# Kernel tuning notes

Hardware: AMD Instinct MI355X
Metric: run time of the kernel (lower is better)

## Reference

```python
import jax, jax.numpy as jnp
import numpy as np
import math

jax.config.update("jax_enable_x64", True)

# cfg constants
N = 4096
DIM = 16
SA = 2.0        # sigma_a
SR = 0.5        # sigma_r
V_SCALE = 1.0
R_H = 6.0
TAU_H = 0.5
K0_KUR = 0.05
TAU_KUR = 2.0
EPS = 1e-7      # acosh clamp epsilon (K=1 curvature)
D_MIN = 0.08    # distance floor in pairwise_dist


def setup_inputs() -> dict:
    key = jax.random.key(0)
    d_star = SA * SR / (SA - SR) * math.log(SA / SR)
    r_init = 0.5 * d_star
    hs = jax.random.normal(key, (N, DIM), dtype=jnp.float64) * r_init
    ht = jnp.sqrt(1.0 + jnp.sum(hs ** 2, axis=-1, keepdims=True))
    h = jnp.concatenate([ht, hs], axis=-1)  # [N, DIM+1] on the hyperboloid
    return {"h": h}


def reference(h):
    """Pairwise hyperbolic distance -> LJ coupling K_geo -> Lorentz-log force F,
    plus LJ potential energy E. Matmul form: no [N,N,dim+1] intermediates."""
    n1 = h.shape[-1]
    metric = jnp.concatenate([-jnp.ones((1,), h.dtype), jnp.ones((n1 - 1,), h.dtype)])
    # Lorentz inner products for all pairs: [N, N] (fp64)
    inn = (h * metric) @ h.T
    # geodesic distance d = acosh(clamp(-<hi,hj>_L, 1+eps))  (K = 1)
    D = jnp.arccosh(jnp.clip(-inn, 1.0 + EPS))
    eye = jnp.eye(N, dtype=h.dtype)
    # exact pairwise_dist semantics: zero diag, add D_MIN to off-diag entries < D_MIN
    D_pair = D * (1.0 - eye) + D_MIN * (((D < D_MIN) & (eye < 0.5)).astype(h.dtype))

    # _build_K in float32 (K_local == 1 since use_dyn_curv=False, learn_K=False)
    D_f = D_pair.astype(jnp.float32)
    eye32 = eye.astype(jnp.float32)
    D_eff = jnp.clip(D_f, 0.05)  # (D / sqrt(clamp(Ki*Kj,1e-4))).clamp(min=0.05) with K_local=1
    dVdd = jnp.exp(-D_eff / SR) / SR - jnp.exp(-D_eff / SA) / SA
    K_geo = -dVdd * V_SCALE * (1.0 - eye32)
    K_geo = K_geo * jax.nn.sigmoid((R_H - D_eff) / TAU_H)  # causal horizon
    K_kur = K0_KUR * jnp.exp(-D_f / TAU_KUR) * (1.0 - eye32)

    # _force: F_i = sum_j K_geo_ij * log_{h_i}(h_j)
    # log_x(y) = d / sqrt(<x,y>^2 - 1) * (y + <x,y> x)
    denom = jnp.sqrt(jnp.clip(inn ** 2 - 1.0, 1e-15))
    C = K_geo.astype(h.dtype) * D / denom  # [N, N]; diag is 0 since K_geo diag is 0
    F = C @ h + jnp.sum(C * inn, axis=-1, keepdims=True) * h  # [N, DIM+1]
    F_norm = jnp.clip(jnp.linalg.norm(F, axis=-1, keepdims=True), 1e-8)
    F = F * jnp.minimum(6.0 / F_norm, 1.0)

    # lj_potential energy on D_pair
    V = V_SCALE * (jnp.exp(-D_pair / SA) - jnp.exp(-D_pair / SR))
    E = jnp.sum(V * (1.0 - eye)) * 0.5
    return F, E
```

## Files before the change

kernel.cpp:

```cpp
#include <hip/hip_runtime.h>

#define NPTS 4096
#define DIMP 17
#define ROWP 20
#define JPB  256
#define NSLAB (NPTS / JPB)
#define NIB   (NPTS / 64)
#define EOFF  (NSLAB * NPTS * ROWP)
#define NEP   (NIB * NSLAB)
#define EDIAG 445.0126f

typedef float v2f __attribute__((ext_vector_type(2)));
typedef float v4f __attribute__((ext_vector_type(4)));

__global__ __launch_bounds__(256, 4) void hydra_pair_kernel(
    const float* __restrict__ h, float* __restrict__ ws,
    float* __restrict__ out, const int use_ws) {
    const int tid   = threadIdx.x;
    const int lane  = tid & 63;
    const int wid   = tid >> 6;
    const int i     = blockIdx.x * 64 + lane;
    const int jbase = blockIdx.y * JPB;

    __shared__ __align__(16) float lds[JPB * ROWP + 8];

#pragma unroll
    for (int kk = 0; kk < DIMP; ++kk) {
        const int idx = tid + kk * 256;
        const int j = idx / DIMP;
        const int k = idx - j * DIMP;
        lds[j * ROWP + k] = h[jbase * DIMP + idx];
    }

    float hraw[DIMP];
#pragma unroll
    for (int k = 0; k < DIMP; ++k) hraw[k] = h[i * DIMP + k];
    v2f hi2[8];
#pragma unroll
    for (int p = 0; p < 8; ++p) { hi2[p].x = hraw[2 * p]; hi2[p].y = hraw[2 * p + 1]; }
    hi2[0].x = -hi2[0].x;
    const float hi16 = hraw[16];

    __syncthreads();

    v2f acc2[8];
#pragma unroll
    for (int p = 0; p < 8; ++p) acc2[p] = (v2f)(0.0f);
    float acc16 = 0.0f;
    float sacc  = 0.0f;
    float eacc  = 0.0f;

    const float* rowp = lds + wid * 64 * ROWP;
#pragma unroll 2
    for (int jj = 0; jj < JPB / 4; ++jj, rowp += ROWP) {
        const v4f a0 = ((const v4f*)rowp)[0];
        const v4f a1 = ((const v4f*)rowp)[1];
        const v4f a2 = ((const v4f*)rowp)[2];
        const v4f a3 = ((const v4f*)rowp)[3];
        const float a16 = rowp[16];
        v2f b[8];
        b[0].x = a0.x; b[0].y = a0.y;  b[1].x = a0.z; b[1].y = a0.w;
        b[2].x = a1.x; b[2].y = a1.y;  b[3].x = a1.z; b[3].y = a1.w;
        b[4].x = a2.x; b[4].y = a2.y;  b[5].x = a2.z; b[5].y = a2.w;
        b[6].x = a3.x; b[6].y = a3.y;  b[7].x = a3.z; b[7].y = a3.w;

        v2f c0 = hi2[0] * b[0];
        v2f c1 = hi2[1] * b[1];
        c0 = __builtin_elementwise_fma(hi2[2], b[2], c0);
        c1 = __builtin_elementwise_fma(hi2[3], b[3], c1);
        c0 = __builtin_elementwise_fma(hi2[4], b[4], c0);
        c1 = __builtin_elementwise_fma(hi2[5], b[5], c1);
        c0 = __builtin_elementwise_fma(hi2[6], b[6], c0);
        c1 = __builtin_elementwise_fma(hi2[7], b[7], c1);
        const v2f cs = c0 + c1;
        const float g = fmaf(hi16, a16, cs.x + cs.y);

        const float x  = fmaxf(-1.0f - g, 1e-7f);
        const float s2 = x * (x + 2.0f);
        const float r  = __builtin_amdgcn_rsqf(s2);
        const float sq = s2 * r;
        const float w  = (x - sq) + 1.0f;
        const float d  = -__logf(w);

        const float fac = (d < 0.08f) ? 0.96078944f : 1.0f;
        const float t = __builtin_amdgcn_sqrtf(w) * fac;
        float u = t * t; u = u * u;
        const float sig = u * __builtin_amdgcn_rcpf(u + 6.1442123533e-6f);
        const float K   = fmaf(0.5f, t, -2.0f * u) * sig;
        const float C   = K * d * r;

        eacc += (t - u);
        sacc = fmaf(C, g, sacc);
        const v2f C2 = {C, C};
#pragma unroll
        for (int p = 0; p < 8; ++p)
            acc2[p] = __builtin_elementwise_fma(C2, b[p], acc2[p]);
        acc16 = fmaf(C, a16, acc16);
    }

    const v2f s2v = {sacc, sacc};
#pragma unroll
    for (int p = 1; p < 8; ++p)
        acc2[p] = __builtin_elementwise_fma(s2v, hi2[p], acc2[p]);
    acc2[0].x = fmaf(-sacc, hi2[0].x, acc2[0].x);
    acc2[0].y = fmaf( sacc, hi2[0].y, acc2[0].y);
    acc16 = fmaf(sacc, hi16, acc16);

#pragma unroll
    for (int off = 32; off > 0; off >>= 1) eacc += __shfl_xor(eacc, off);

    __syncthreads();
    if (wid > 0) {
        float* dst = lds + ((wid - 1) * 64 + lane) * ROWP;
#pragma unroll
        for (int p = 0; p < 8; ++p) ((v2f*)dst)[p] = acc2[p];
        dst[16] = acc16;
    }
    if (lane == 0 && wid > 0) lds[JPB * ROWP + wid] = eacc;
    __syncthreads();

    if (wid == 0) {
        const float esum = eacc + lds[JPB * ROWP + 1] + lds[JPB * ROWP + 2] +
                           lds[JPB * ROWP + 3];
#pragma unroll
        for (int q = 0; q < 3; ++q) {
            const float* src = lds + (q * 64 + lane) * ROWP;
#pragma unroll
            for (int p = 0; p < 8; ++p) acc2[p] += ((const v2f*)src)[p];
            acc16 += src[16];
        }
        if (use_ws) {
            float* dst = ws + ((size_t)blockIdx.y * NPTS + i) * ROWP;
#pragma unroll
            for (int p = 0; p < 8; ++p) ((v2f*)dst)[p] = acc2[p];
            dst[16] = acc16;
            if (lane == 0) ws[EOFF + blockIdx.y * NIB + blockIdx.x] = esum;
        } else {
#pragma unroll
            for (int p = 0; p < 8; ++p) {
                atomicAdd(&out[i * DIMP + 2 * p],     acc2[p].x);
                atomicAdd(&out[i * DIMP + 2 * p + 1], acc2[p].y);
            }
            atomicAdd(&out[i * DIMP + 16], acc16);
            if (lane == 0) atomicAdd(&out[NPTS * DIMP], esum);
        }
    }
}

__global__ __launch_bounds__(256) void hydra_finalize_kernel(
    const float* __restrict__ ws, float* __restrict__ out, const int use_ws) {
    const int tid  = threadIdx.x;
    const int lane = tid & 63;
    const int q    = tid >> 6;
    const int i    = blockIdx.x * 64 + lane;

    __shared__ __align__(16) float red[3 * 64 * ROWP + 8];

    float v[DIMP];
#pragma unroll
    for (int k = 0; k < DIMP; ++k) v[k] = 0.0f;

    if (use_ws) {
#pragma unroll
        for (int ss = 0; ss < NSLAB / 4; ++ss) {
            const int s = q * (NSLAB / 4) + ss;
            const float* row = ws + ((size_t)s * NPTS + i) * ROWP;
            const v4f b0 = ((const v4f*)row)[0];
            const v4f b1 = ((const v4f*)row)[1];
            const v4f b2 = ((const v4f*)row)[2];
            const v4f b3 = ((const v4f*)row)[3];
            v[0]  += b0.x; v[1]  += b0.y; v[2]  += b0.z; v[3]  += b0.w;
            v[4]  += b1.x; v[5]  += b1.y; v[6]  += b1.z; v[7]  += b1.w;
            v[8]  += b2.x; v[9]  += b2.y; v[10] += b2.z; v[11] += b2.w;
            v[12] += b3.x; v[13] += b3.y; v[14] += b3.z; v[15] += b3.w;
            v[16] += row[16];
        }
        if (q > 0) {
            float* dst = red + ((q - 1) * 64 + lane) * ROWP;
#pragma unroll
            for (int k = 0; k < DIMP; ++k) dst[k] = v[k];
        }
        __syncthreads();
        if (q == 0) {
#pragma unroll
            for (int qq = 0; qq < 3; ++qq) {
                const float* src = red + (qq * 64 + lane) * ROWP;
#pragma unroll
                for (int k = 0; k < DIMP; ++k) v[k] += src[k];
            }
        }
    } else if (q == 0) {
#pragma unroll
        for (int k = 0; k < DIMP; ++k) v[k] = out[i * DIMP + k];
    }

    if (q == 0) {
        float ss = 0.0f;
#pragma unroll
        for (int k = 0; k < DIMP; ++k) ss = fmaf(v[k], v[k], ss);
        const float nrm   = sqrtf(ss);
        const float scale = fminf(6.0f / fmaxf(nrm, 1e-8f), 1.0f);
#pragma unroll
        for (int k = 0; k < DIMP; ++k) out[i * DIMP + k] = v[k] * scale;
    }

    if (blockIdx.x == 0) {
        if (use_ws) {
            float e = 0.0f;
#pragma unroll
            for (int t = 0; t < NEP / 256; ++t) e += ws[EOFF + tid + t * 256];
#pragma unroll
            for (int off = 32; off > 0; off >>= 1) e += __shfl_xor(e, off);
            __shared__ float es[4];
            if (lane == 0) es[q] = e;
            __syncthreads();
            if (tid == 0)
                out[NPTS * DIMP] = 0.5f * ((es[0] + es[1] + es[2] + es[3]) - EDIAG);
        } else {
            if (tid == 0) out[NPTS * DIMP] = 0.5f * (out[NPTS * DIMP] - EDIAG);
        }
    }
}

extern "C" void kernel_launch(void* const* d_in, const int* in_sizes, int n_in,
                              void* d_out, int out_size, void* d_ws, size_t ws_size,
                              hipStream_t stream) {
    const float* h = (const float*)d_in[0];
    float* out = (float*)d_out;
    float* ws  = (float*)d_ws;

    const size_t need = (size_t)(EOFF + NEP) * sizeof(float);
    const int use_ws = (ws_size >= need) ? 1 : 0;
    if (!use_ws) {
        hipMemsetAsync(d_out, 0, (size_t)out_size * sizeof(float), stream);
    }

    dim3 grid(NIB, NSLAB);
    hydra_pair_kernel<<<grid, 256, 0, stream>>>(h, ws, out, use_ws);
    hydra_finalize_kernel<<<64, 256, 0, stream>>>(ws, out, use_ws);
}
```

Measured before the change: 39.03 us.

## Split each pair block across eight waves and prefetch next LDS row

```diff
diff --git a/kernel.cpp b/kernel.cpp
--- a/kernel.cpp
+++ b/kernel.cpp
@@ -9,11 +9,12 @@
 #define EOFF  (NSLAB * NPTS * ROWP)
 #define NEP   (NIB * NSLAB)
 #define EDIAG 445.0126f
+#define REDROWS (7 * 64)
 
 typedef float v2f __attribute__((ext_vector_type(2)));
 typedef float v4f __attribute__((ext_vector_type(4)));
 
-__global__ __launch_bounds__(256, 4) void hydra_pair_kernel(
+__global__ __launch_bounds__(512) void hydra_pair_kernel(
     const float* __restrict__ h, float* __restrict__ ws,
     float* __restrict__ out, const int use_ws) {
     const int tid   = threadIdx.x;
@@ -22,11 +23,9 @@
     const int i     = blockIdx.x * 64 + lane;
     const int jbase = blockIdx.y * JPB;
 
-    __shared__ __align__(16) float lds[JPB * ROWP + 8];
-
-#pragma unroll
-    for (int kk = 0; kk < DIMP; ++kk) {
-        const int idx = tid + kk * 256;
+    __shared__ __align__(16) float lds[REDROWS * ROWP + 16];
+
+    for (int idx = tid; idx < JPB * DIMP; idx += 512) {
         const int j = idx / DIMP;
         const int k = idx - j * DIMP;
         lds[j * ROWP + k] = h[jbase * DIMP + idx];
@@ -50,28 +49,32 @@
     float sacc  = 0.0f;
     float eacc  = 0.0f;
 
-    const float* rowp = lds + wid * 64 * ROWP;
+    const float* rowp = lds + (wid * 32) * ROWP;
+    v4f n0 = ((const v4f*)rowp)[0];
+    v4f n1 = ((const v4f*)rowp)[1];
+    v4f n2 = ((const v4f*)rowp)[2];
+    v4f n3 = ((const v4f*)rowp)[3];
+    float n16 = rowp[16];
+
 #pragma unroll 2
-    for (int jj = 0; jj < JPB / 4; ++jj, rowp += ROWP) {
-        const v4f a0 = ((const v4f*)rowp)[0];
-        const v4f a1 = ((const v4f*)rowp)[1];
-        const v4f a2 = ((const v4f*)rowp)[2];
-        const v4f a3 = ((const v4f*)rowp)[3];
-        const float a16 = rowp[16];
-        v2f b[8];
-        b[0].x = a0.x; b[0].y = a0.y;  b[1].x = a0.z; b[1].y = a0.w;
-        b[2].x = a1.x; b[2].y = a1.y;  b[3].x = a1.z; b[3].y = a1.w;
-        b[4].x = a2.x; b[4].y = a2.y;  b[5].x = a2.z; b[5].y = a2.w;
-        b[6].x = a3.x; b[6].y = a3.y;  b[7].x = a3.z; b[7].y = a3.w;
-
-        v2f c0 = hi2[0] * b[0];
-        v2f c1 = hi2[1] * b[1];
-        c0 = __builtin_elementwise_fma(hi2[2], b[2], c0);
-        c1 = __builtin_elementwise_fma(hi2[3], b[3], c1);
-        c0 = __builtin_elementwise_fma(hi2[4], b[4], c0);
-        c1 = __builtin_elementwise_fma(hi2[5], b[5], c1);
-        c0 = __builtin_elementwise_fma(hi2[6], b[6], c0);
-        c1 = __builtin_elementwise_fma(hi2[7], b[7], c1);
+    for (int jj = 0; jj < 32; ++jj) {
+        const v4f a0 = n0, a1 = n1, a2 = n2, a3 = n3;
+        const float a16 = n16;
+        rowp += ROWP;
+        n0 = ((const v4f*)rowp)[0];
+        n1 = ((const v4f*)rowp)[1];
+        n2 = ((const v4f*)rowp)[2];
+        n3 = ((const v4f*)rowp)[3];
+        n16 = rowp[16];
+
+        v2f c0 = hi2[0] * a0.lo;
+        v2f c1 = hi2[1] * a0.hi;
+        c0 = __builtin_elementwise_fma(hi2[2], a1.lo, c0);
+        c1 = __builtin_elementwise_fma(hi2[3], a1.hi, c1);
+        c0 = __builtin_elementwise_fma(hi2[4], a2.lo, c0);
+        c1 = __builtin_elementwise_fma(hi2[5], a2.hi, c1);
+        c0 = __builtin_elementwise_fma(hi2[6], a3.lo, c0);
+        c1 = __builtin_elementwise_fma(hi2[7], a3.hi, c1);
         const v2f cs = c0 + c1;
         const float g = fmaf(hi16, a16, cs.x + cs.y);
 
@@ -92,9 +95,14 @@
         eacc += (t - u);
         sacc = fmaf(C, g, sacc);
         const v2f C2 = {C, C};
-#pragma unroll
-        for (int p = 0; p < 8; ++p)
-            acc2[p] = __builtin_elementwise_fma(C2, b[p], acc2[p]);
+        acc2[0] = __builtin_elementwise_fma(C2, a0.lo, acc2[0]);
+        acc2[1] = __builtin_elementwise_fma(C2, a0.hi, acc2[1]);
+        acc2[2] = __builtin_elementwise_fma(C2, a1.lo, acc2[2]);
+        acc2[3] = __builtin_elementwise_fma(C2, a1.hi, acc2[3]);
+        acc2[4] = __builtin_elementwise_fma(C2, a2.lo, acc2[4]);
+        acc2[5] = __builtin_elementwise_fma(C2, a2.hi, acc2[5]);
+        acc2[6] = __builtin_elementwise_fma(C2, a3.lo, acc2[6]);
+        acc2[7] = __builtin_elementwise_fma(C2, a3.hi, acc2[7]);
         acc16 = fmaf(C, a16, acc16);
     }
 
@@ -116,14 +124,15 @@
         for (int p = 0; p < 8; ++p) ((v2f*)dst)[p] = acc2[p];
         dst[16] = acc16;
     }
-    if (lane == 0 && wid > 0) lds[JPB * ROWP + wid] = eacc;
+    if (lane == 0) lds[REDROWS * ROWP + wid] = eacc;
     __syncthreads();
 
     if (wid == 0) {
-        const float esum = eacc + lds[JPB * ROWP + 1] + lds[JPB * ROWP + 2] +
-                           lds[JPB * ROWP + 3];
-#pragma unroll
-        for (int q = 0; q < 3; ++q) {
+        float esum = 0.0f;
+#pragma unroll
+        for (int q = 0; q < 8; ++q) esum += lds[REDROWS * ROWP + q];
+#pragma unroll
+        for (int q = 0; q < 7; ++q) {
             const float* src = lds + (q * 64 + lane) * ROWP;
 #pragma unroll
             for (int p = 0; p < 8; ++p) acc2[p] += ((const v2f*)src)[p];
@@ -236,6 +245,6 @@
     }
 
     dim3 grid(NIB, NSLAB);
-    hydra_pair_kernel<<<grid, 256, 0, stream>>>(h, ws, out, use_ws);
+    hydra_pair_kernel<<<grid, 512, 0, stream>>>(h, ws, out, use_ws);
     hydra_finalize_kernel<<<64, 256, 0, stream>>>(ws, out, use_ws);
 }
```

Result: no change. 39.00 us (-0.1%).

## Register-block two query rows per thread and simplify pair math

Applied to the files above, without the earlier changes.

```diff
diff --git a/kernel.cpp b/kernel.cpp
--- a/kernel.cpp
+++ b/kernel.cpp
@@ -3,12 +3,14 @@
 #define NPTS 4096
 #define DIMP 17
 #define ROWP 20
-#define JPB  256
+#define RROW 21
+#define JPB  128
+#define IPB  128
 #define NSLAB (NPTS / JPB)
-#define NIB   (NPTS / 64)
+#define NIB   (NPTS / IPB)
 #define EOFF  (NSLAB * NPTS * ROWP)
 #define NEP   (NIB * NSLAB)
-#define EDIAG 445.0126f
+#define REDF  (384 * RROW)
 
 typedef float v2f __attribute__((ext_vector_type(2)));
 typedef float v4f __attribute__((ext_vector_type(4)));
@@ -19,129 +21,131 @@
     const int tid   = threadIdx.x;
     const int lane  = tid & 63;
     const int wid   = tid >> 6;
-    const int i     = blockIdx.x * 64 + lane;
+    const int i0    = blockIdx.x * IPB;
+    const int i1    = i0 + lane;
+    const int i2    = i0 + 64 + lane;
     const int jbase = blockIdx.y * JPB;
 
-    __shared__ __align__(16) float lds[JPB * ROWP + 8];
-
-#pragma unroll
-    for (int kk = 0; kk < DIMP; ++kk) {
-        const int idx = tid + kk * 256;
+    __shared__ __align__(16) float lds[REDF + 16];
+
+    for (int idx = tid; idx < JPB * DIMP; idx += 256) {
         const int j = idx / DIMP;
         const int k = idx - j * DIMP;
         lds[j * ROWP + k] = h[jbase * DIMP + idx];
     }
 
-    float hraw[DIMP];
-#pragma unroll
-    for (int k = 0; k < DIMP; ++k) hraw[k] = h[i * DIMP + k];
-    v2f hi2[8];
-#pragma unroll
-    for (int p = 0; p < 8; ++p) { hi2[p].x = hraw[2 * p]; hi2[p].y = hraw[2 * p + 1]; }
-    hi2[0].x = -hi2[0].x;
-    const float hi16 = hraw[16];
+    float nh1[DIMP], nh2[DIMP];
+#pragma unroll
+    for (int k = 0; k < DIMP; ++k) nh1[k] = -h[i1 * DIMP + k];
+#pragma unroll
+    for (int k = 0; k < DIMP; ++k) nh2[k] = -h[i2 * DIMP + k];
+    nh1[0] = -nh1[0];
+    nh2[0] = -nh2[0];
 
     __syncthreads();
 
-    v2f acc2[8];
-#pragma unroll
-    for (int p = 0; p < 8; ++p) acc2[p] = (v2f)(0.0f);
-    float acc16 = 0.0f;
-    float sacc  = 0.0f;
-    float eacc  = 0.0f;
-
-    const float* rowp = lds + wid * 64 * ROWP;
+    float ac1[DIMP], ac2[DIMP];
+#pragma unroll
+    for (int k = 0; k < DIMP; ++k) { ac1[k] = 0.0f; ac2[k] = 0.0f; }
+    float sm1 = 0.0f, sm2 = 0.0f;
+    float eacc = 0.0f;
+
+    const float* rowp = lds + (wid * 32) * ROWP;
 #pragma unroll 2
-    for (int jj = 0; jj < JPB / 4; ++jj, rowp += ROWP) {
+    for (int jj = 0; jj < 32; ++jj, rowp += ROWP) {
         const v4f a0 = ((const v4f*)rowp)[0];
         const v4f a1 = ((const v4f*)rowp)[1];
         const v4f a2 = ((const v4f*)rowp)[2];
         const v4f a3 = ((const v4f*)rowp)[3];
         const float a16 = rowp[16];
-        v2f b[8];
-        b[0].x = a0.x; b[0].y = a0.y;  b[1].x = a0.z; b[1].y = a0.w;
-        b[2].x = a1.x; b[2].y = a1.y;  b[3].x = a1.z; b[3].y = a1.w;
-        b[4].x = a2.x; b[4].y = a2.y;  b[5].x = a2.z; b[5].y = a2.w;
-        b[6].x = a3.x; b[6].y = a3.y;  b[7].x = a3.z; b[7].y = a3.w;
-
-        v2f c0 = hi2[0] * b[0];
-        v2f c1 = hi2[1] * b[1];
-        c0 = __builtin_elementwise_fma(hi2[2], b[2], c0);
-        c1 = __builtin_elementwise_fma(hi2[3], b[3], c1);
-        c0 = __builtin_elementwise_fma(hi2[4], b[4], c0);
-        c1 = __builtin_elementwise_fma(hi2[5], b[5], c1);
-        c0 = __builtin_elementwise_fma(hi2[6], b[6], c0);
-        c1 = __builtin_elementwise_fma(hi2[7], b[7], c1);
-        const v2f cs = c0 + c1;
-        const float g = fmaf(hi16, a16, cs.x + cs.y);
-
-        const float x  = fmaxf(-1.0f - g, 1e-7f);
-        const float s2 = x * (x + 2.0f);
-        const float r  = __builtin_amdgcn_rsqf(s2);
-        const float sq = s2 * r;
-        const float w  = (x - sq) + 1.0f;
-        const float d  = -__logf(w);
-
-        const float fac = (d < 0.08f) ? 0.96078944f : 1.0f;
-        const float t = __builtin_amdgcn_sqrtf(w) * fac;
-        float u = t * t; u = u * u;
-        const float sig = u * __builtin_amdgcn_rcpf(u + 6.1442123533e-6f);
-        const float K   = fmaf(0.5f, t, -2.0f * u) * sig;
-        const float C   = K * d * r;
-
-        eacc += (t - u);
-        sacc = fmaf(C, g, sacc);
-        const v2f C2 = {C, C};
-#pragma unroll
-        for (int p = 0; p < 8; ++p)
-            acc2[p] = __builtin_elementwise_fma(C2, b[p], acc2[p]);
-        acc16 = fmaf(C, a16, acc16);
-    }
-
-    const v2f s2v = {sacc, sacc};
-#pragma unroll
-    for (int p = 1; p < 8; ++p)
-        acc2[p] = __builtin_elementwise_fma(s2v, hi2[p], acc2[p]);
-    acc2[0].x = fmaf(-sacc, hi2[0].x, acc2[0].x);
-    acc2[0].y = fmaf( sacc, hi2[0].y, acc2[0].y);
-    acc16 = fmaf(sacc, hi16, acc16);
+        const float hj[DIMP] = {a0.x, a0.y, a0.z, a0.w, a1.x, a1.y, a1.z, a1.w,
+                                a2.x, a2.y, a2.z, a2.w, a3.x, a3.y, a3.z, a3.w, a16};
+
+        float p0 = nh1[0] * hj[0], p1 = nh1[1] * hj[1];
+        float q0 = nh2[0] * hj[0], q1 = nh2[1] * hj[1];
+#pragma unroll
+        for (int k = 2; k < 16; k += 2) {
+            p0 = fmaf(nh1[k], hj[k], p0);     p1 = fmaf(nh1[k + 1], hj[k + 1], p1);
+            q0 = fmaf(nh2[k], hj[k], q0);     q1 = fmaf(nh2[k + 1], hj[k + 1], q1);
+        }
+        const float m1 = fmaf(nh1[16], a16, p0 + p1);
+        const float m2 = fmaf(nh2[16], a16, q0 + q1);
+
+        const float x1  = m1 - 1.0f;
+        const float ss1 = fmaxf(fmaf(m1, m1, -1.0f), 2e-7f);
+        const float r1  = __builtin_amdgcn_rsqf(ss1);
+        const float sq1 = ss1 * r1;
+        const float w1  = (x1 - sq1) + 1.0f;
+        const float d1  = -__logf(w1);
+        const float t1  = __builtin_amdgcn_sqrtf(w1);
+        const float u1  = w1 * w1;
+        const float g1  = u1 * __builtin_amdgcn_rcpf(u1 + 6.1442123533e-6f);
+        const float K1  = fmaf(0.5f, t1, -2.0f * u1) * g1;
+        const float C1  = K1 * d1 * r1;
+        const float x2  = m2 - 1.0f;
+        const float ss2 = fmaxf(fmaf(m2, m2, -1.0f), 2e-7f);
+        const float r2  = __builtin_amdgcn_rsqf(ss2);
+        const float sq2 = ss2 * r2;
+        const float w2  = (x2 - sq2) + 1.0f;
+        const float d2  = -__logf(w2);
+        const float t2  = __builtin_amdgcn_sqrtf(w2);
+        const float u2  = w2 * w2;
+        const float g2  = u2 * __builtin_amdgcn_rcpf(u2 + 6.1442123533e-6f);
+        const float K2  = fmaf(0.5f, t2, -2.0f * u2) * g2;
+        const float C2  = K2 * d2 * r2;
+
+        eacc += (t1 - u1) + (t2 - u2);
+        sm1 = fmaf(C1, m1, sm1);
+        sm2 = fmaf(C2, m2, sm2);
+#pragma unroll
+        for (int k = 0; k < DIMP; ++k) {
+            ac1[k] = fmaf(C1, hj[k], ac1[k]);
+            ac2[k] = fmaf(C2, hj[k], ac2[k]);
+        }
+    }
+
+    ac1[0] = fmaf(-sm1, nh1[0], ac1[0]);
+    ac2[0] = fmaf(-sm2, nh2[0], ac2[0]);
+#pragma unroll
+    for (int k = 1; k < DIMP; ++k) {
+        ac1[k] = fmaf(sm1, nh1[k], ac1[k]);
+        ac2[k] = fmaf(sm2, nh2[k], ac2[k]);
+    }
 
 #pragma unroll
     for (int off = 32; off > 0; off >>= 1) eacc += __shfl_xor(eacc, off);
 
     __syncthreads();
     if (wid > 0) {
-        float* dst = lds + ((wid - 1) * 64 + lane) * ROWP;
-#pragma unroll
-        for (int p = 0; p < 8; ++p) ((v2f*)dst)[p] = acc2[p];
-        dst[16] = acc16;
-    }
-    if (lane == 0 && wid > 0) lds[JPB * ROWP + wid] = eacc;
+        float* dA = lds + ((wid - 1) * 64 + lane) * RROW;
+        float* dB = lds + ((192 + (wid - 1) * 64 + lane)) * RROW;
+#pragma unroll
+        for (int k = 0; k < DIMP; ++k) { dA[k] = ac1[k]; dB[k] = ac2[k]; }
+        if (lane == 0) lds[REDF + wid] = eacc;
+    }
     __syncthreads();
 
     if (wid == 0) {
-        const float esum = eacc + lds[JPB * ROWP + 1] + lds[JPB * ROWP + 2] +
-                           lds[JPB * ROWP + 3];
+        const float esum = eacc + lds[REDF + 1] + lds[REDF + 2] + lds[REDF + 3];
 #pragma unroll
         for (int q = 0; q < 3; ++q) {
-            const float* src = lds + (q * 64 + lane) * ROWP;
-#pragma unroll
-            for (int p = 0; p < 8; ++p) acc2[p] += ((const v2f*)src)[p];
-            acc16 += src[16];
+            const float* sA = lds + (q * 64 + lane) * RROW;
+            const float* sB = lds + ((192 + q * 64 + lane)) * RROW;
+#pragma unroll
+            for (int k = 0; k < DIMP; ++k) { ac1[k] += sA[k]; ac2[k] += sB[k]; }
         }
         if (use_ws) {
-            float* dst = ws + ((size_t)blockIdx.y * NPTS + i) * ROWP;
-#pragma unroll
-            for (int p = 0; p < 8; ++p) ((v2f*)dst)[p] = acc2[p];
-            dst[16] = acc16;
+            float* w1p = ws + ((size_t)blockIdx.y * NPTS + i1) * ROWP;
+            float* w2p = ws + ((size_t)blockIdx.y * NPTS + i2) * ROWP;
+#pragma unroll
+            for (int k = 0; k < DIMP; ++k) { w1p[k] = ac1[k]; w2p[k] = ac2[k]; }
             if (lane == 0) ws[EOFF + blockIdx.y * NIB + blockIdx.x] = esum;
         } else {
 #pragma unroll
-            for (int p = 0; p < 8; ++p) {
-                atomicAdd(&out[i * DIMP + 2 * p],     acc2[p].x);
-                atomicAdd(&out[i * DIMP + 2 * p + 1], acc2[p].y);
+            for (int k = 0; k < DIMP; ++k) {
+                atomicAdd(&out[i1 * DIMP + k], ac1[k]);
+                atomicAdd(&out[i2 * DIMP + k], ac2[k]);
             }
-            atomicAdd(&out[i * DIMP + 16], acc16);
             if (lane == 0) atomicAdd(&out[NPTS * DIMP], esum);
         }
     }
@@ -154,7 +158,7 @@
     const int q    = tid >> 6;
     const int i    = blockIdx.x * 64 + lane;
 
-    __shared__ __align__(16) float red[3 * 64 * ROWP + 8];
+    __shared__ __align__(16) float red[3 * 64 * RROW + 8];
 
     float v[DIMP];
 #pragma unroll
@@ -162,8 +166,8 @@
 
     if (use_ws) {
 #pragma unroll
-        for (int ss = 0; ss < NSLAB / 4; ++ss) {
-            const int s = q * (NSLAB / 4) + ss;
+        for (int ssl = 0; ssl < NSLAB / 4; ++ssl) {
+            const int s = q * (NSLAB / 4) + ssl;
             const float* row = ws + ((size_t)s * NPTS + i) * ROWP;
             const v4f b0 = ((const v4f*)row)[0];
             const v4f b1 = ((const v4f*)row)[1];
@@ -176,7 +180,7 @@
             v[16] += row[16];
         }
         if (q > 0) {
-            float* dst = red + ((q - 1) * 64 + lane) * ROWP;
+            float* dst = red + ((q - 1) * 64 + lane) * RROW;
 #pragma unroll
             for (int k = 0; k < DIMP; ++k) dst[k] = v[k];
         }
@@ -184,7 +188,7 @@
         if (q == 0) {
 #pragma unroll
             for (int qq = 0; qq < 3; ++qq) {
-                const float* src = red + (qq * 64 + lane) * ROWP;
+                const float* src = red + (qq * 64 + lane) * RROW;
 #pragma unroll
                 for (int k = 0; k < DIMP; ++k) v[k] += src[k];
             }
@@ -214,10 +218,9 @@
             __shared__ float es[4];
             if (lane == 0) es[q] = e;
             __syncthreads();
-            if (tid == 0)
-                out[NPTS * DIMP] = 0.5f * ((es[0] + es[1] + es[2] + es[3]) - EDIAG);
+            if (tid == 0) out[NPTS * DIMP] = 0.5f * (es[0] + es[1] + es[2] + es[3]);
         } else {
-            if (tid == 0) out[NPTS * DIMP] = 0.5f * (out[NPTS * DIMP] - EDIAG);
+            if (tid == 0) out[NPTS * DIMP] *= 0.5f;
         }
     }
 }
```

After: 44.18 us. 1.13x slower.
